# Kernel optimization log

Measured on AMD Instinct MI355X. Metric: run time of the kernel, lower is better.

## Reference

```python
import jax, jax.numpy as jnp
import numpy as np
from jax import lax

K = 3          # kernel_size
G = 2          # num_groups
DN = ('NHWC', 'HWIO', 'NHWC')


def _conv_same(x, w, b, groups=1):
    y = lax.conv_general_dilated(x, w, (1, 1), 'SAME',
                                 dimension_numbers=DN,
                                 feature_group_count=groups)
    return y + b


def _kernel_grid():
    off = (K - 1) / 2.0
    lin = jnp.linspace(-off, off, K, dtype=jnp.float32)
    dx, dy = jnp.meshgrid(lin, lin)              # 'xy' indexing, like tf default
    return jnp.stack([dx, dy], axis=-1).reshape(K * K, 2)  # [K2, 2] (dx, dy)


def _bilinear_sample(inp, loc):
    # inp: [B,H,W,C], loc: [B,H,W,K2,2] with (x,y) already clipped to valid range
    B, H, W, C = inp.shape
    x, y = loc[..., 0], loc[..., 1]
    x0 = jnp.floor(x); y0 = jnp.floor(y)
    x1 = jnp.clip(x0 + 1.0, 0.0, W - 1.0); x0 = jnp.clip(x0, 0.0, W - 1.0)
    y1 = jnp.clip(y0 + 1.0, 0.0, H - 1.0); y0 = jnp.clip(y0, 0.0, H - 1.0)
    # corner weights (computed from clipped coords, matching the TF code)
    wa = (x1 - x) * (y1 - y)
    wb = (x1 - x) * (y - y0)
    wc = (x - x0) * (y1 - y)
    wd = (x - x0) * (y - y0)
    x0i = x0.astype(jnp.int32); x1i = x1.astype(jnp.int32)
    y0i = y0.astype(jnp.int32); y1i = y1.astype(jnp.int32)
    flat = inp.reshape(B, H * W, C)

    def gather(yi, xi):
        idx = (yi * W + xi).reshape(B, -1, 1)               # [B, H*W*K2, 1]
        v = jnp.take_along_axis(flat, idx, axis=1)          # [B, H*W*K2, C]
        return v.reshape(B, H, W, K * K, C)

    out = (wa[..., None] * gather(y0i, x0i) + wb[..., None] * gather(y1i, x0i)
           + wc[..., None] * gather(y0i, x1i) + wd[..., None] * gather(y1i, x1i))
    return out  # [B,H,W,K2,C]


def _forward(x, off_w, off_b, dw_w, dw_b, pw_w, pw_b):
    B, H, W, C = x.shape
    Cg = C // G
    kg = _kernel_grid()                                     # [K2,2]
    gx, gy = jnp.meshgrid(jnp.arange(W, dtype=jnp.float32),
                          jnp.arange(H, dtype=jnp.float32))
    grid = jnp.stack([gx, gy], axis=-1)                     # [H,W,2] (x,y)
    outs = []
    for g in range(G):
        xi = x[..., g * Cg:(g + 1) * Cg]                    # [B,H,W,Cg]
        offsets = _conv_same(xi, off_w[g], off_b[g])        # [B,H,W,2*K2]
        offsets = offsets.reshape(B, H, W, K * K, 2)
        loc = grid[None, :, :, None, :] + kg[None, None, None] + offsets
        loc = jnp.stack([jnp.clip(loc[..., 0], 0.0, W - 1.0),
                         jnp.clip(loc[..., 1], 0.0, H - 1.0)], axis=-1)
        sampled = _bilinear_sample(xi, loc)                 # [B,H,W,K2,Cg]
        Kin = K * K * Cg
        s = sampled.reshape(B, H, W, Kin)
        s = _conv_same(s, dw_w[g], dw_b[g], groups=Kin)     # depthwise 3x3
        s = _conv_same(s, pw_w[g], pw_b[g])                 # 1x1 pointwise
        outs.append(s)
    return jnp.concatenate(outs, axis=-1)


def setup_inputs() -> dict:
    key = jax.random.key(0)
    ks = jax.random.split(key, 6)
    B, H, W, C = 4, 128, 128, 128
    Cg = C // G
    F = 128
    Fg = F // G
    Kin = K * K * Cg
    x = jax.random.normal(ks[0], (B, H, W, C), jnp.float32)
    # offset conv (zero-init in source; small random weights so offsets ~1px)
    off_w = jax.random.normal(ks[1], (G, K, K, Cg, 2 * K * K), jnp.float32) * 0.05
    off_b = jnp.zeros((G, 2 * K * K), jnp.float32)
    dw_w = jax.random.normal(ks[2], (G, K, K, 1, Kin), jnp.float32) * 0.1
    dw_b = jnp.zeros((G, Kin), jnp.float32)
    pw_w = jax.random.normal(ks[3], (G, 1, 1, Kin, Fg), jnp.float32) / np.sqrt(Kin)
    pw_b = jnp.zeros((G, Fg), jnp.float32)
    return {"x": x, "off_w": off_w, "off_b": off_b,
            "dw_w": dw_w, "dw_b": dw_b, "pw_w": pw_w, "pw_b": pw_b}


def reference(x, off_w, off_b, dw_w, dw_b, pw_w, pw_b):
    return _forward(x, off_w, off_b, dw_w, dw_b, pw_w, pw_b)
```

## Files before the change

kernel.cpp:

```cpp
#include <hip/hip_runtime.h>
#include <hip/hip_bf16.h>

#define HW 128
#define GNUM 2
#define BATCH 4
#define BHW2 (BATCH * HW * HW)
#define OFF_WS_FLOATS (GNUM * 18 * BHW2)
#define OBT_STRIDE (GNUM * 18 * 2 * 512)
#define PWT_FLOATS 36864
#define OBT_FLOATS 36864

typedef short s16x8 __attribute__((ext_vector_type(8)));
typedef float f32x4 __attribute__((ext_vector_type(4)));

__device__ inline unsigned short f2bf(float f) {
    union { float f; unsigned u; } v;
    v.f = f;
    unsigned r = (v.u + 0x7fffu + ((v.u >> 16) & 1u)) >> 16;
    return (unsigned short)r;
}
__device__ inline unsigned pk2bf(float lo, float hi) {
    __hip_bfloat162 r = __float22bfloat162_rn(float2{lo, hi});
    return *(unsigned*)&r;
}
__device__ inline float blo(unsigned u) {
    union { unsigned u; float f; } v; v.u = u << 16; return v.f;
}
__device__ inline float bhi(unsigned u) {
    union { unsigned u; float f; } v; v.u = u & 0xffff0000u; return v.f;
}

__global__ __launch_bounds__(256) void prep_kernel(
    const float* __restrict__ pw_w, const float* __restrict__ dw_b,
    const float* __restrict__ off_w, unsigned short* __restrict__ pwt,
    unsigned short* __restrict__ obt, float* __restrict__ bias2) {
    const int g = blockIdx.y;
    const int t = threadIdx.x;
    if (blockIdx.x < 9) {
        const int j = blockIdx.x;
        const int wv = t >> 6, lane = t & 63;
        const int f = wv * 16 + (lane & 15);
        const int kbase = (lane >> 4) << 3;
        float part = 0.f;
#pragma unroll
        for (int ks = 0; ks < 2; ++ks)
#pragma unroll
            for (int i = 0; i < 8; ++i) {
                int kin = j * 64 + ks * 32 + kbase + i;
                float v = pw_w[(g * 576 + kin) * 64 + f];
                pwt[((((g * 9 + j) * 4 + wv) * 2 + ks) << 9) + lane * 8 + i] =
                    f2bf(v);
                part += v * dw_b[g * 576 + kin];
            }
        atomicAdd(&bias2[g * 64 + f], part);
    } else {
        const int s = blockIdx.x - 9;
        const int tap = s >> 1;
        for (int e = t; e < 1024; e += 256) {
            int nt = e >> 9, le = e & 511;
            int lane = le >> 3, i = le & 7;
            int k = ((lane >> 4) << 3) + i;
            int c = ((s & 1) << 5) + k;
            int n = (nt << 4) + (lane & 15);
            float v = (n < 18) ? off_w[((g * 9 + tap) * 64 + c) * 18 + n] : 0.f;
            unsigned short hi = f2bf(v);
            unsigned short lo = f2bf(v - blo(hi));
            int idx = (((g * 18 + s) * 2 + nt) << 9) + le;
            obt[idx] = hi;
            obt[OBT_STRIDE + idx] = lo;
        }
    }
}

__global__ __launch_bounds__(256) void offset_mfma(
    const float* __restrict__ x, const unsigned short* __restrict__ obt,
    const float* __restrict__ off_b, float* __restrict__ off_ws) {
    __shared__ unsigned short xh[100 * 72];
    const int b = blockIdx.x >> 1, g = blockIdx.x & 1;
    const int tileIdx = blockIdx.y;
    const int h0 = (tileIdx >> 4) << 3, w0 = (tileIdx & 15) << 3;
    const int t = threadIdx.x;
    const int lane = t & 63;
    const int wv = __builtin_amdgcn_readfirstlane(t >> 6);
    const int m = (wv << 4) + (lane & 15);
    const int pyy = m >> 3, pxx = m & 7;
    const int kq = (lane >> 4) << 3;

    f32x4 acc[2];
    {
        const int col = lane & 15;
        float b0 = (col < 18) ? off_b[g * 18 + col] : 0.f;
        float b1 = (col + 16 < 18) ? off_b[g * 18 + col + 16] : 0.f;
        acc[0] = (f32x4){b0, b0, b0, b0};
        acc[1] = (f32x4){b1, b1, b1, b1};
    }
    for (int q = 0; q < 2; ++q) {
        if (q) __syncthreads();
        for (int idx = t; idx < 800; idx += 256) {
            int sp = idx >> 3, cq = idx & 7;
            int sy = sp / 10, sx = sp - sy * 10;
            int gy = h0 - 1 + sy, gx = w0 - 1 + sx;
            uint2 hp = {0, 0}, lp = {0, 0};
            if ((unsigned)gy < HW && (unsigned)gx < HW) {
                const float4 v = *(const float4*)&x[(((b * HW + gy) * HW + gx)
                                                    << 7) +
                                                   (g << 6) + (q << 5) + (cq << 2)];
                hp.x = pk2bf(v.x, v.y);
                hp.y = pk2bf(v.z, v.w);
                lp.x = pk2bf(v.x - blo(hp.x), v.y - bhi(hp.x));
                lp.y = pk2bf(v.z - blo(hp.y), v.w - bhi(hp.y));
            }
            *(uint2*)&xh[sp * 72 + (cq << 2)] = hp;
            *(uint2*)&xh[sp * 72 + 32 + (cq << 2)] = lp;
        }
        __syncthreads();
        for (int tap = 0; tap < 9; ++tap) {
            const int s = (tap << 1) + q;
            const int ky = tap / 3, kx = tap - ky * 3;
            const int bidx = ((g * 18 + s) << 1) << 9;
            s16x8 bh0 = *(const s16x8*)&obt[bidx + lane * 8];
            s16x8 bh1 = *(const s16x8*)&obt[bidx + 512 + lane * 8];
            s16x8 bl0 = *(const s16x8*)&obt[OBT_STRIDE + bidx + lane * 8];
            s16x8 bl1 = *(const s16x8*)&obt[OBT_STRIDE + bidx + 512 + lane * 8];
            const int base = ((pyy + ky) * 10 + pxx + kx) * 72;
            s16x8 ah = *(const s16x8*)&xh[base + kq];
            s16x8 al = *(const s16x8*)&xh[base + 32 + kq];
            acc[0] = __builtin_amdgcn_mfma_f32_16x16x32_bf16(ah, bh0, acc[0],
                                                             0, 0, 0);
            acc[1] = __builtin_amdgcn_mfma_f32_16x16x32_bf16(ah, bh1, acc[1],
                                                             0, 0, 0);
            acc[0] = __builtin_amdgcn_mfma_f32_16x16x32_bf16(al, bh0, acc[0],
                                                             0, 0, 0);
            acc[1] = __builtin_amdgcn_mfma_f32_16x16x32_bf16(al, bh1, acc[1],
                                                             0, 0, 0);
            acc[0] = __builtin_amdgcn_mfma_f32_16x16x32_bf16(ah, bl0, acc[0],
                                                             0, 0, 0);
            acc[1] = __builtin_amdgcn_mfma_f32_16x16x32_bf16(ah, bl1, acc[1],
                                                             0, 0, 0);
        }
    }
    const int col = lane & 15;
    const int rq = (lane >> 4) << 2;
    const int m0 = (wv << 4) + rq;
    const int pixrow = b * (HW * HW) + (h0 + (m0 >> 3)) * HW + w0 + (m0 & 7);
#pragma unroll
    for (int nt = 0; nt < 2; ++nt) {
        int o = (nt << 4) + col;
        if (o < 18)
            *(f32x4*)&off_ws[(g * 18 + o) * BHW2 + pixrow] = acc[nt];
    }
}

__global__ __launch_bounds__(256, 6) void deform_kernel(
    const float* __restrict__ x, const float* __restrict__ off_ws,
    const float* __restrict__ dw_w, const unsigned short* __restrict__ pwt,
    const float* __restrict__ bias2, const float* __restrict__ pw_b,
    float* __restrict__ out) {
    __shared__ unsigned short samp[100 * 72];
    __shared__ unsigned short dwa[64 * 72];
    __shared__ float4 wlw[100];
    __shared__ int4 wli[100];
    const int b = blockIdx.x >> 1, g = blockIdx.x & 1;
    const int tileIdx = blockIdx.y;
    const int h0 = (tileIdx >> 4) << 3, w0 = (tileIdx & 15) << 3;
    const int t = threadIdx.x;
    const int lane = t & 63;
    const int wv = __builtin_amdgcn_readfirstlane(t >> 6);
    const int fb = wv << 4;
    const int p = lane;
    const int ayp = p >> 3, axp = p & 7;
    const int grp = t >> 4, sl = t & 15;

    const float bs = bias2[g * 64 + fb + (lane & 15)] +
                     pw_b[g * 64 + fb + (lane & 15)];
    f32x4 acc[4];
#pragma unroll
    for (int mt = 0; mt < 4; ++mt) acc[mt] = (f32x4){bs, bs, bs, bs};

    for (int j = 0; j < 9; ++j) {
        const int jy = j / 3, jx = j - jy * 3;
        s16x8 bfr[2];
#pragma unroll
        for (int ks = 0; ks < 2; ++ks)
            bfr[ks] = *(const s16x8*)&pwt[((((g * 9 + j) * 4 + wv) * 2 + ks)
                                           << 9) + lane * 8];
        if (t < 100) {
            const int sp = t;
            const int spy = sp / 10, spx = sp - spy * 10;
            const int gy = h0 - 1 + spy, gx = w0 - 1 + spx;
            float4 w4 = {0.f, 0.f, 0.f, 0.f};
            int4 ii = {b << 21, 0, 0, 0};
            if ((unsigned)gy < HW && (unsigned)gx < HW) {
                const int pix = b * (HW * HW) + gy * HW + gx;
                const float ox = off_ws[(g * 18 + 2 * j) * BHW2 + pix];
                const float oy = off_ws[(g * 18 + 2 * j + 1) * BHW2 + pix];
                float xf = fminf(fmaxf((float)(gx + jx - 1) + ox, 0.f), 127.f);
                float yf = fminf(fmaxf((float)(gy + jy - 1) + oy, 0.f), 127.f);
                float x0 = floorf(xf), y0 = floorf(yf);
                float x1 = fminf(x0 + 1.f, 127.f);
                float y1 = fminf(y0 + 1.f, 127.f);
                w4.x = (x1 - xf) * (y1 - yf);
                w4.y = (x1 - xf) * (yf - y0);
                w4.z = (xf - x0) * (y1 - yf);
                w4.w = (xf - x0) * (yf - y0);
                const int x0i = (int)x0, y0i = (int)y0;
                ii.x = ((b * HW + y0i) * HW + x0i) << 7;
                ii.y = ((int)x1 - x0i) << 7;
                ii.z = ((int)y1 - y0i) << 14;
            }
            wlw[sp] = w4;
            wli[sp] = ii;
        }
        __syncthreads();
        for (int it = 0; it < 7; ++it) {
            const int sp = (it << 4) + grp;
            if (sp < 100) {
                const float4 w4 = wlw[sp];
                const int4 ii = wli[sp];
                const float* xa = x + ii.x + (g << 6) + (sl << 2);
                const float4 va = *(const float4*)xa;
                const float4 vb = *(const float4*)(xa + ii.z);
                const float4 vc = *(const float4*)(xa + ii.y);
                const float4 vd = *(const float4*)(xa + ii.y + ii.z);
                float r0 = w4.x * va.x + w4.y * vb.x + w4.z * vc.x + w4.w * vd.x;
                float r1 = w4.x * va.y + w4.y * vb.y + w4.z * vc.y + w4.w * vd.y;
                float r2 = w4.x * va.z + w4.y * vb.z + w4.z * vc.z + w4.w * vd.z;
                float r3 = w4.x * va.w + w4.y * vb.w + w4.z * vc.w + w4.w * vd.w;
                uint2 pk;
                pk.x = pk2bf(r0, r1);
                pk.y = pk2bf(r2, r3);
                *(uint2*)&samp[sp * 72 + (sl << 2)] = pk;
            }
        }
        __syncthreads();
#pragma unroll
        for (int cq = 0; cq < 2; ++cq) {
            const int c8 = fb + (cq << 3);
            float d0 = 0.f, d1 = 0.f, d2 = 0.f, d3 = 0.f;
            float d4 = 0.f, d5 = 0.f, d6 = 0.f, d7 = 0.f;
#pragma unroll
            for (int ky = 0; ky < 3; ++ky)
#pragma unroll
                for (int kx = 0; kx < 3; ++kx) {
                    const uint4 hv = *(const uint4*)&samp
                        [((ayp + ky) * 10 + axp + kx) * 72 + c8];
                    const float* wr =
                        &dw_w[((g * 3 + ky) * 3 + kx) * 576 + (j << 6) + c8];
                    d0 += blo(hv.x) * wr[0]; d1 += bhi(hv.x) * wr[1];
                    d2 += blo(hv.y) * wr[2]; d3 += bhi(hv.y) * wr[3];
                    d4 += blo(hv.z) * wr[4]; d5 += bhi(hv.z) * wr[5];
                    d6 += blo(hv.w) * wr[6]; d7 += bhi(hv.w) * wr[7];
                }
            uint4 pk;
            pk.x = pk2bf(d0, d1);
            pk.y = pk2bf(d2, d3);
            pk.z = pk2bf(d4, d5);
            pk.w = pk2bf(d6, d7);
            *(uint4*)&dwa[p * 72 + c8] = pk;
        }
        __syncthreads();
#pragma unroll
        for (int ks = 0; ks < 2; ++ks)
#pragma unroll
            for (int mt = 0; mt < 4; ++mt) {
                s16x8 af = *(const s16x8*)&dwa[(mt * 16 + (lane & 15)) * 72 +
                                               ks * 32 + ((lane >> 4) << 3)];
                acc[mt] = __builtin_amdgcn_mfma_f32_16x16x32_bf16(
                    af, bfr[ks], acc[mt], 0, 0, 0);
            }
    }
    const int col = lane & 15;
    const int rq = (lane >> 4) << 2;
#pragma unroll
    for (int mt = 0; mt < 4; ++mt)
#pragma unroll
        for (int i = 0; i < 4; ++i) {
            int m = mt * 16 + rq + i;
            out[((b * HW + h0 + (m >> 3)) * HW + (w0 + (m & 7))) * 128 +
                (g << 6) + fb + col] = acc[mt][i];
        }
}

extern "C" void kernel_launch(void* const* d_in, const int* in_sizes, int n_in,
                              void* d_out, int out_size, void* d_ws,
                              size_t ws_size, hipStream_t stream) {
    const float* x = (const float*)d_in[0];
    const float* off_w = (const float*)d_in[1];
    const float* off_b = (const float*)d_in[2];
    const float* dw_w = (const float*)d_in[3];
    const float* dw_b = (const float*)d_in[4];
    const float* pw_w = (const float*)d_in[5];
    const float* pw_b = (const float*)d_in[6];

    float* wsf = (float*)d_ws;
    float* off_ws = wsf;
    unsigned short* pwt =
        (unsigned short*)(wsf + OFF_WS_FLOATS);
    unsigned short* obt =
        (unsigned short*)(wsf + OFF_WS_FLOATS + PWT_FLOATS);
    float* bias2 = wsf + OFF_WS_FLOATS + PWT_FLOATS + OBT_FLOATS;

    hipMemsetAsync(bias2, 0, GNUM * 64 * sizeof(float), stream);
    prep_kernel<<<dim3(27, GNUM), dim3(256), 0, stream>>>(pw_w, dw_b, off_w,
                                                          pwt, obt, bias2);
    offset_mfma<<<dim3(BATCH * GNUM, 256), dim3(256), 0, stream>>>(
        x, obt, off_b, off_ws);
    deform_kernel<<<dim3(BATCH * GNUM, 256), dim3(256), 0, stream>>>(
        x, off_ws, dw_w, pwt, bias2, pw_b, (float*)d_out);
}
```

Before: 215.5 us.

## Fuse offset convolution into deformable sampling kernel via halo recompute

```diff
diff --git a/kernel.cpp b/kernel.cpp
--- a/kernel.cpp
+++ b/kernel.cpp
@@ -4,8 +4,6 @@
 #define HW 128
 #define GNUM 2
 #define BATCH 4
-#define BHW2 (BATCH * HW * HW)
-#define OFF_WS_FLOATS (GNUM * 18 * BHW2)
 #define OBT_STRIDE (GNUM * 18 * 2 * 512)
 #define PWT_FLOATS 36864
 #define OBT_FLOATS 36864
@@ -72,34 +70,51 @@
     }
 }
 
-__global__ __launch_bounds__(256) void offset_mfma(
+__global__ __launch_bounds__(256, 4) void deform_fused(
     const float* __restrict__ x, const unsigned short* __restrict__ obt,
-    const float* __restrict__ off_b, float* __restrict__ off_ws) {
-    __shared__ unsigned short xh[100 * 72];
+    const float* __restrict__ off_b, const float* __restrict__ dw_w,
+    const unsigned short* __restrict__ pwt, const float* __restrict__ bias2,
+    const float* __restrict__ pw_b, float* __restrict__ out) {
+    __shared__ char smem[34016];
+    unsigned short* xh = (unsigned short*)smem;
+    unsigned short* samp = (unsigned short*)smem;
+    unsigned short* dwa = (unsigned short*)(smem + 14400);
+    float* offs = (float*)(smem + 23616);
+    float4* wlw = (float4*)(smem + 30816);
+    int4* wli = (int4*)(smem + 32416);
+
     const int b = blockIdx.x >> 1, g = blockIdx.x & 1;
     const int tileIdx = blockIdx.y;
     const int h0 = (tileIdx >> 4) << 3, w0 = (tileIdx & 15) << 3;
     const int t = threadIdx.x;
     const int lane = t & 63;
     const int wv = __builtin_amdgcn_readfirstlane(t >> 6);
-    const int m = (wv << 4) + (lane & 15);
-    const int pyy = m >> 3, pxx = m & 7;
     const int kq = (lane >> 4) << 3;
-
-    f32x4 acc[2];
-    {
-        const int col = lane & 15;
-        float b0 = (col < 18) ? off_b[g * 18 + col] : 0.f;
-        float b1 = (col + 16 < 18) ? off_b[g * 18 + col + 16] : 0.f;
-        acc[0] = (f32x4){b0, b0, b0, b0};
-        acc[1] = (f32x4){b1, b1, b1, b1};
+    const int col = lane & 15;
+    const int rq = (lane >> 4) << 2;
+
+    f32x4 oacc[2][2];
+#pragma unroll
+    for (int sl = 0; sl < 2; ++sl)
+#pragma unroll
+        for (int nt = 0; nt < 2; ++nt) oacc[sl][nt] = (f32x4){0.f, 0.f, 0.f, 0.f};
+    int mbase[2];
+#pragma unroll
+    for (int sl = 0; sl < 2; ++sl) {
+        int mt = wv + (sl << 2);
+        int m = mt * 16 + col;
+        if (mt < 7 && m < 100) {
+            int opy = m / 10, opx = m - opy * 10;
+            mbase[sl] = opy * 12 + opx;
+        } else
+            mbase[sl] = 0;
     }
     for (int q = 0; q < 2; ++q) {
         if (q) __syncthreads();
-        for (int idx = t; idx < 800; idx += 256) {
+        for (int idx = t; idx < 144 * 8; idx += 256) {
             int sp = idx >> 3, cq = idx & 7;
-            int sy = sp / 10, sx = sp - sy * 10;
-            int gy = h0 - 1 + sy, gx = w0 - 1 + sx;
+            int sy = sp / 12, sx = sp - sy * 12;
+            int gy = h0 - 2 + sy, gx = w0 - 2 + sx;
             uint2 hp = {0, 0}, lp = {0, 0};
             if ((unsigned)gy < HW && (unsigned)gx < HW) {
                 const float4 v = *(const float4*)&x[(((b * HW + gy) * HW + gx)
@@ -117,62 +132,60 @@
         for (int tap = 0; tap < 9; ++tap) {
             const int s = (tap << 1) + q;
             const int ky = tap / 3, kx = tap - ky * 3;
+            const int shift = ky * 12 + kx;
             const int bidx = ((g * 18 + s) << 1) << 9;
             s16x8 bh0 = *(const s16x8*)&obt[bidx + lane * 8];
             s16x8 bh1 = *(const s16x8*)&obt[bidx + 512 + lane * 8];
             s16x8 bl0 = *(const s16x8*)&obt[OBT_STRIDE + bidx + lane * 8];
             s16x8 bl1 = *(const s16x8*)&obt[OBT_STRIDE + bidx + 512 + lane * 8];
-            const int base = ((pyy + ky) * 10 + pxx + kx) * 72;
-            s16x8 ah = *(const s16x8*)&xh[base + kq];
-            s16x8 al = *(const s16x8*)&xh[base + 32 + kq];
-            acc[0] = __builtin_amdgcn_mfma_f32_16x16x32_bf16(ah, bh0, acc[0],
-                                                             0, 0, 0);
-            acc[1] = __builtin_amdgcn_mfma_f32_16x16x32_bf16(ah, bh1, acc[1],
-                                                             0, 0, 0);
-            acc[0] = __builtin_amdgcn_mfma_f32_16x16x32_bf16(al, bh0, acc[0],
-                                                             0, 0, 0);
-            acc[1] = __builtin_amdgcn_mfma_f32_16x16x32_bf16(al, bh1, acc[1],
-                                                             0, 0, 0);
-            acc[0] = __builtin_amdgcn_mfma_f32_16x16x32_bf16(ah, bl0, acc[0],
-                                                             0, 0, 0);
-            acc[1] = __builtin_amdgcn_mfma_f32_16x16x32_bf16(ah, bl1, acc[1],
-                                                             0, 0, 0);
-        }
-    }
-    const int col = lane & 15;
-    const int rq = (lane >> 4) << 2;
-    const int m0 = (wv << 4) + rq;
-    const int pixrow = b * (HW * HW) + (h0 + (m0 >> 3)) * HW + w0 + (m0 & 7);
-#pragma unroll
-    for (int nt = 0; nt < 2; ++nt) {
-        int o = (nt << 4) + col;
-        if (o < 18)
-            *(f32x4*)&off_ws[(g * 18 + o) * BHW2 + pixrow] = acc[nt];
-    }
-}
-
-__global__ __launch_bounds__(256, 6) void deform_kernel(
-    const float* __restrict__ x, const float* __restrict__ off_ws,
-    const float* __restrict__ dw_w, const unsigned short* __restrict__ pwt,
-    const float* __restrict__ bias2, const float* __restrict__ pw_b,
-    float* __restrict__ out) {
-    __shared__ unsigned short samp[100 * 72];
-    __shared__ unsigned short dwa[64 * 72];
-    __shared__ float4 wlw[100];
-    __shared__ int4 wli[100];
-    const int b = blockIdx.x >> 1, g = blockIdx.x & 1;
-    const int tileIdx = blockIdx.y;
-    const int h0 = (tileIdx >> 4) << 3, w0 = (tileIdx & 15) << 3;
-    const int t = threadIdx.x;
-    const int lane = t & 63;
-    const int wv = __builtin_amdgcn_readfirstlane(t >> 6);
+#pragma unroll
+            for (int sl = 0; sl < 2; ++sl) {
+                if (wv + (sl << 2) < 7) {
+                    const int base2 = (mbase[sl] + shift) * 72 + kq;
+                    s16x8 ah = *(const s16x8*)&xh[base2];
+                    s16x8 al = *(const s16x8*)&xh[base2 + 32];
+                    oacc[sl][0] = __builtin_amdgcn_mfma_f32_16x16x32_bf16(
+                        ah, bh0, oacc[sl][0], 0, 0, 0);
+                    oacc[sl][1] = __builtin_amdgcn_mfma_f32_16x16x32_bf16(
+                        ah, bh1, oacc[sl][1], 0, 0, 0);
+                    oacc[sl][0] = __builtin_amdgcn_mfma_f32_16x16x32_bf16(
+                        al, bh0, oacc[sl][0], 0, 0, 0);
+                    oacc[sl][1] = __builtin_amdgcn_mfma_f32_16x16x32_bf16(
+                        al, bh1, oacc[sl][1], 0, 0, 0);
+                    oacc[sl][0] = __builtin_amdgcn_mfma_f32_16x16x32_bf16(
+                        ah, bl0, oacc[sl][0], 0, 0, 0);
+                    oacc[sl][1] = __builtin_amdgcn_mfma_f32_16x16x32_bf16(
+                        ah, bl1, oacc[sl][1], 0, 0, 0);
+                }
+            }
+        }
+    }
+#pragma unroll
+    for (int sl = 0; sl < 2; ++sl) {
+        int mt = wv + (sl << 2);
+        if (mt < 7) {
+#pragma unroll
+            for (int nt = 0; nt < 2; ++nt) {
+                int o = (nt << 4) + col;
+                if (o < 18) {
+                    float ob = off_b[g * 18 + o];
+#pragma unroll
+                    for (int i = 0; i < 4; ++i) {
+                        int m = mt * 16 + rq + i;
+                        if (m < 100) offs[m * 18 + o] = oacc[sl][nt][i] + ob;
+                    }
+                }
+            }
+        }
+    }
+    __syncthreads();
+
     const int fb = wv << 4;
     const int p = lane;
     const int ayp = p >> 3, axp = p & 7;
-    const int grp = t >> 4, sl = t & 15;
-
-    const float bs = bias2[g * 64 + fb + (lane & 15)] +
-                     pw_b[g * 64 + fb + (lane & 15)];
+    const int grp = t >> 4, sl16 = t & 15;
+
+    const float bs = bias2[g * 64 + fb + col] + pw_b[g * 64 + fb + col];
     f32x4 acc[4];
 #pragma unroll
     for (int mt = 0; mt < 4; ++mt) acc[mt] = (f32x4){bs, bs, bs, bs};
@@ -191,9 +204,8 @@
             float4 w4 = {0.f, 0.f, 0.f, 0.f};
             int4 ii = {b << 21, 0, 0, 0};
             if ((unsigned)gy < HW && (unsigned)gx < HW) {
-                const int pix = b * (HW * HW) + gy * HW + gx;
-                const float ox = off_ws[(g * 18 + 2 * j) * BHW2 + pix];
-                const float oy = off_ws[(g * 18 + 2 * j + 1) * BHW2 + pix];
+                const float ox = offs[sp * 18 + 2 * j];
+                const float oy = offs[sp * 18 + 2 * j + 1];
                 float xf = fminf(fmaxf((float)(gx + jx - 1) + ox, 0.f), 127.f);
                 float yf = fminf(fmaxf((float)(gy + jy - 1) + oy, 0.f), 127.f);
                 float x0 = floorf(xf), y0 = floorf(yf);
@@ -217,7 +229,7 @@
             if (sp < 100) {
                 const float4 w4 = wlw[sp];
                 const int4 ii = wli[sp];
-                const float* xa = x + ii.x + (g << 6) + (sl << 2);
+                const float* xa = x + ii.x + (g << 6) + (sl16 << 2);
                 const float4 va = *(const float4*)xa;
                 const float4 vb = *(const float4*)(xa + ii.z);
                 const float4 vc = *(const float4*)(xa + ii.y);
@@ -229,7 +241,7 @@
                 uint2 pk;
                 pk.x = pk2bf(r0, r1);
                 pk.y = pk2bf(r2, r3);
-                *(uint2*)&samp[sp * 72 + (sl << 2)] = pk;
+                *(uint2*)&samp[sp * 72 + (sl16 << 2)] = pk;
             }
         }
         __syncthreads();
@@ -263,14 +275,12 @@
         for (int ks = 0; ks < 2; ++ks)
 #pragma unroll
             for (int mt = 0; mt < 4; ++mt) {
-                s16x8 af = *(const s16x8*)&dwa[(mt * 16 + (lane & 15)) * 72 +
-                                               ks * 32 + ((lane >> 4) << 3)];
+                s16x8 af = *(const s16x8*)&dwa[(mt * 16 + col) * 72 + ks * 32 +
+                                               kq];
                 acc[mt] = __builtin_amdgcn_mfma_f32_16x16x32_bf16(
                     af, bfr[ks], acc[mt], 0, 0, 0);
             }
     }
-    const int col = lane & 15;
-    const int rq = (lane >> 4) << 2;
 #pragma unroll
     for (int mt = 0; mt < 4; ++mt)
 #pragma unroll
@@ -293,18 +303,13 @@
     const float* pw_b = (const float*)d_in[6];
 
     float* wsf = (float*)d_ws;
-    float* off_ws = wsf;
-    unsigned short* pwt =
-        (unsigned short*)(wsf + OFF_WS_FLOATS);
-    unsigned short* obt =
-        (unsigned short*)(wsf + OFF_WS_FLOATS + PWT_FLOATS);
-    float* bias2 = wsf + OFF_WS_FLOATS + PWT_FLOATS + OBT_FLOATS;
+    unsigned short* pwt = (unsigned short*)wsf;
+    unsigned short* obt = (unsigned short*)(wsf + PWT_FLOATS);
+    float* bias2 = wsf + PWT_FLOATS + OBT_FLOATS;
 
     hipMemsetAsync(bias2, 0, GNUM * 64 * sizeof(float), stream);
     prep_kernel<<<dim3(27, GNUM), dim3(256), 0, stream>>>(pw_w, dw_b, off_w,
                                                           pwt, obt, bias2);
-    offset_mfma<<<dim3(BATCH * GNUM, 256), dim3(256), 0, stream>>>(
-        x, obt, off_b, off_ws);
-    deform_kernel<<<dim3(BATCH * GNUM, 256), dim3(256), 0, stream>>>(
-        x, off_ws, dw_w, pwt, bias2, pw_b, (float*)d_out);
-}
+    deform_fused<<<dim3(BATCH * GNUM, 256), dim3(256), 0, stream>>>(
+        x, obt, off_b, dw_w, pwt, bias2, pw_b, (float*)d_out);
+}
```

After: 207.1 us. 1.04x faster.
